# Kernel optimization log

Hardware: AMD Instinct MI355X
Metric: run time of the kernel (lower is better)

The kernel has to match this reference:

```python
import jax, jax.numpy as jnp
import numpy as np

HIDDEN = 64
SEQ_LEN = 50
NUM_ITEM = 40000
BATCH = 1024


def setup_inputs() -> dict:
    key = jax.random.key(0)
    ks = jax.random.split(key, 8)
    all_memory = jax.random.normal(ks[0], (BATCH, SEQ_LEN, HIDDEN), dtype=jnp.float32)
    last_memory = jax.random.normal(ks[1], (BATCH, HIDDEN), dtype=jnp.float32)
    seq_item = jax.random.randint(ks[2], (BATCH, SEQ_LEN), 0, NUM_ITEM)
    # learned params (xavier-ish init)
    s = 1.0 / np.sqrt(HIDDEN)
    Wr = jax.random.normal(ks[3], (HIDDEN, HIDDEN), dtype=jnp.float32) * s
    Ur = jax.random.normal(ks[4], (HIDDEN, HIDDEN), dtype=jnp.float32) * s
    Vr_w = jax.random.normal(ks[5], (HIDDEN,), dtype=jnp.float32) * s
    Vr_b = jnp.zeros((), dtype=jnp.float32)
    return {"all_memory": all_memory, "last_memory": last_memory,
            "seq_item": seq_item, "Wr": Wr, "Ur": Ur, "Vr_w": Vr_w, "Vr_b": Vr_b}


def reference(all_memory, last_memory, seq_item, Wr, Ur, Vr_w, Vr_b):
    # Dropout is identity in eval mode.
    a = jnp.einsum('bsh,kh->bsk', all_memory, Ur)        # Ur(all_memory)
    l = jnp.einsum('bh,kh->bk', last_memory, Wr)          # Wr(last_memory)
    h = jnp.tanh(a + l[:, None, :])                       # [B, S, H]
    scores = jnp.einsum('bsh,h->bs', h, Vr_w) + Vr_b      # Vr(.) -> [B, S]
    probs = jax.nn.softmax(scores, axis=-1)               # [B, S]
    # Scatter-add seq-level probs into vocab (equiv. to matmul with one-hot map;
    # duplicate items within a sequence accumulate, matching the dense matmul).
    B = probs.shape[0]
    out = jnp.zeros((B, NUM_ITEM), dtype=probs.dtype)
    out = out.at[jnp.arange(B)[:, None], seq_item].add(probs)
    return out
```

## Files before the change

kernel.cpp:

```cpp
#include <hip/hip_runtime.h>
#include <math.h>

constexpr int B = 1024;
constexpr int S = 50;
constexpr int H = 64;
constexpr int V = 40000;

__global__ __launch_bounds__(256) void rrd_zero_kernel(float4* __restrict__ out4)
{
    const size_t n4     = (size_t)B * V / 4;
    const size_t stride = (size_t)gridDim.x * 256;
    size_t i = (size_t)blockIdx.x * 256 + threadIdx.x;
    const float4 z = make_float4(0.f, 0.f, 0.f, 0.f);
    for (; i < n4; i += stride) out4[i] = z;
}

__global__ __launch_bounds__(256) void rrd_compute_kernel(
    const float* __restrict__ am,
    const float* __restrict__ lm,
    const int*   __restrict__ items,
    const float* __restrict__ Wr,
    const float* __restrict__ Ur,
    const float* __restrict__ Vw,
    const float* __restrict__ Vb,
    float* __restrict__ out)
{
    const int b    = blockIdx.x;
    const int tid  = threadIdx.x;
    const int lane = tid & 63;
    const int wave = tid >> 6;

    __shared__ float s_l[H];
    __shared__ float s_sc[S];

    if (tid < H) {
        const float4* wr4 = reinterpret_cast<const float4*>(Wr + tid * H);
        const float4* l4  = reinterpret_cast<const float4*>(lm + (size_t)b * H);
        float acc = 0.f;
        #pragma unroll
        for (int i = 0; i < H / 4; ++i) {
            float4 w = wr4[i], x = l4[i];
            acc = fmaf(x.x, w.x, acc);
            acc = fmaf(x.y, w.y, acc);
            acc = fmaf(x.z, w.z, acc);
            acc = fmaf(x.w, w.w, acc);
        }
        s_l[tid] = acc;
    }

    float ur[H];
    {
        const float4* u4 = reinterpret_cast<const float4*>(Ur + lane * H);
        #pragma unroll
        for (int i = 0; i < H / 4; ++i) {
            float4 u = u4[i];
            ur[4 * i + 0] = u.x;
            ur[4 * i + 1] = u.y;
            ur[4 * i + 2] = u.z;
            ur[4 * i + 3] = u.w;
        }
    }
    const float vw = Vw[lane];
    __syncthreads();
    const float lk = s_l[lane];

    for (int s = wave; s < S; s += 4) {
        const float4* a4 =
            reinterpret_cast<const float4*>(am + ((size_t)b * S + s) * H);
        float acc = lk;
        #pragma unroll
        for (int i = 0; i < H / 4; ++i) {
            float4 v = a4[i];
            acc = fmaf(v.x, ur[4 * i + 0], acc);
            acc = fmaf(v.y, ur[4 * i + 1], acc);
            acc = fmaf(v.z, ur[4 * i + 2], acc);
            acc = fmaf(v.w, ur[4 * i + 3], acc);
        }
        float t = tanhf(acc) * vw;
        #pragma unroll
        for (int off = 32; off; off >>= 1) t += __shfl_xor(t, off, 64);
        if (lane == 0) s_sc[s] = t + Vb[0];
    }
    __syncthreads();

    if (wave == 0) {
        float x = (lane < S) ? s_sc[lane] : -INFINITY;
        float m = x;
        #pragma unroll
        for (int off = 32; off; off >>= 1) m = fmaxf(m, __shfl_xor(m, off, 64));
        float e = (lane < S) ? expf(x - m) : 0.f;
        float sum = e;
        #pragma unroll
        for (int off = 32; off; off >>= 1) sum += __shfl_xor(sum, off, 64);
        if (lane < S) {
            const int it = items[b * S + lane];
            atomicAdd(out + (size_t)b * V + it, e / sum);
        }
    }
}

extern "C" void kernel_launch(void* const* d_in, const int* in_sizes, int n_in,
                              void* d_out, int out_size, void* d_ws, size_t ws_size,
                              hipStream_t stream) {
    const float* am    = (const float*)d_in[0];
    const float* lm    = (const float*)d_in[1];
    const int*   items = (const int*)  d_in[2];
    const float* Wr    = (const float*)d_in[3];
    const float* Ur    = (const float*)d_in[4];
    const float* Vw    = (const float*)d_in[5];
    const float* Vb    = (const float*)d_in[6];
    float* out = (float*)d_out;

    rrd_zero_kernel<<<dim3(2048), dim3(256), 0, stream>>>(
        reinterpret_cast<float4*>(out));
    rrd_compute_kernel<<<dim3(B), dim3(256), 0, stream>>>(
        am, lm, items, Wr, Ur, Vw, Vb, out);
}
```

Baseline: 221.6 us.

## Stage sequence rows in LDS, compute Wr projection per lane, use hipMemsetAsync

```diff
diff --git a/kernel.cpp b/kernel.cpp
--- a/kernel.cpp
+++ b/kernel.cpp
@@ -5,17 +5,9 @@
 constexpr int S = 50;
 constexpr int H = 64;
 constexpr int V = 40000;
+constexpr int NRMAX = 13;
 
-__global__ __launch_bounds__(256) void rrd_zero_kernel(float4* __restrict__ out4)
-{
-    const size_t n4     = (size_t)B * V / 4;
-    const size_t stride = (size_t)gridDim.x * 256;
-    size_t i = (size_t)blockIdx.x * 256 + threadIdx.x;
-    const float4 z = make_float4(0.f, 0.f, 0.f, 0.f);
-    for (; i < n4; i += stride) out4[i] = z;
-}
-
-__global__ __launch_bounds__(256) void rrd_compute_kernel(
+__global__ __launch_bounds__(256) void rrd_compute_v2(
     const float* __restrict__ am,
     const float* __restrict__ lm,
     const int*   __restrict__ items,
@@ -29,23 +21,15 @@
     const int tid  = threadIdx.x;
     const int lane = tid & 63;
     const int wave = tid >> 6;
+    const int nr   = (S - wave + 3) >> 2;
 
-    __shared__ float s_l[H];
+    __shared__ float s_am[4][NRMAX * H];
     __shared__ float s_sc[S];
 
-    if (tid < H) {
-        const float4* wr4 = reinterpret_cast<const float4*>(Wr + tid * H);
-        const float4* l4  = reinterpret_cast<const float4*>(lm + (size_t)b * H);
-        float acc = 0.f;
-        #pragma unroll
-        for (int i = 0; i < H / 4; ++i) {
-            float4 w = wr4[i], x = l4[i];
-            acc = fmaf(x.x, w.x, acc);
-            acc = fmaf(x.y, w.y, acc);
-            acc = fmaf(x.z, w.z, acc);
-            acc = fmaf(x.w, w.w, acc);
-        }
-        s_l[tid] = acc;
+    {
+        const float* base = am + ((size_t)b * S + wave) * H + lane;
+        for (int r = 0; r < nr; ++r)
+            s_am[wave][r * H + lane] = base[(size_t)r * 4 * H];
     }
 
     float ur[H];
@@ -54,19 +38,27 @@
         #pragma unroll
         for (int i = 0; i < H / 4; ++i) {
             float4 u = u4[i];
-            ur[4 * i + 0] = u.x;
-            ur[4 * i + 1] = u.y;
-            ur[4 * i + 2] = u.z;
-            ur[4 * i + 3] = u.w;
+            ur[4 * i + 0] = u.x; ur[4 * i + 1] = u.y;
+            ur[4 * i + 2] = u.z; ur[4 * i + 3] = u.w;
+        }
+    }
+    float lk = 0.f;
+    {
+        const float4* w4 = reinterpret_cast<const float4*>(Wr + lane * H);
+        const float4* l4 = reinterpret_cast<const float4*>(lm + (size_t)b * H);
+        #pragma unroll
+        for (int i = 0; i < H / 4; ++i) {
+            float4 w = w4[i], x = l4[i];
+            lk = fmaf(x.x, w.x, lk); lk = fmaf(x.y, w.y, lk);
+            lk = fmaf(x.z, w.z, lk); lk = fmaf(x.w, w.w, lk);
         }
     }
     const float vw = Vw[lane];
-    __syncthreads();
-    const float lk = s_l[lane];
+    const float vb = Vb[0];
+    const int my_item = (tid < S) ? items[b * S + tid] : 0;
 
-    for (int s = wave; s < S; s += 4) {
-        const float4* a4 =
-            reinterpret_cast<const float4*>(am + ((size_t)b * S + s) * H);
+    for (int r = 0; r < nr; ++r) {
+        const float4* a4 = reinterpret_cast<const float4*>(&s_am[wave][r * H]);
         float acc = lk;
         #pragma unroll
         for (int i = 0; i < H / 4; ++i) {
@@ -79,7 +71,7 @@
         float t = tanhf(acc) * vw;
         #pragma unroll
         for (int off = 32; off; off >>= 1) t += __shfl_xor(t, off, 64);
-        if (lane == 0) s_sc[s] = t + Vb[0];
+        if (lane == 0) s_sc[wave + 4 * r] = t + vb;
     }
     __syncthreads();
 
@@ -92,10 +84,8 @@
         float sum = e;
         #pragma unroll
         for (int off = 32; off; off >>= 1) sum += __shfl_xor(sum, off, 64);
-        if (lane < S) {
-            const int it = items[b * S + lane];
-            atomicAdd(out + (size_t)b * V + it, e / sum);
-        }
+        if (lane < S)
+            atomicAdd(out + (size_t)b * V + my_item, e / sum);
     }
 }
 
@@ -111,8 +101,8 @@
     const float* Vb    = (const float*)d_in[6];
     float* out = (float*)d_out;
 
-    rrd_zero_kernel<<<dim3(2048), dim3(256), 0, stream>>>(
-        reinterpret_cast<float4*>(out));
-    rrd_compute_kernel<<<dim3(B), dim3(256), 0, stream>>>(
+    hipMemsetAsync(d_out, 0, (size_t)B * V * sizeof(float), stream);
+
+    rrd_compute_v2<<<dim3(B), dim3(256), 0, stream>>>(
         am, lm, items, Wr, Ur, Vw, Vb, out);
 }
```

New measurement: 208.9 us. -5.7%, faster.
